# Performance work log

Measured on AMD Instinct MI355X. Metric: run time of the kernel, lower is better.

The kernel has to match this reference:

```python
import jax, jax.numpy as jnp
import numpy as np

D_MODEL = 32
SEQ = 128  # input_dim: each scalar feature is a token


def setup_inputs() -> dict:
    key = jax.random.key(0)
    ks = jax.random.split(key, 11)
    B = 16384
    s = 1.0 / np.sqrt(D_MODEL)
    return {
        "x": jax.random.normal(ks[0], (B, SEQ), dtype=jnp.float32),
        "Wt": jax.random.normal(ks[1], (1, D_MODEL), dtype=jnp.float32),  # token_proj weight (in=1)
        "bt": jax.random.normal(ks[2], (D_MODEL,), dtype=jnp.float32) * 0.02,
        "Wq": jax.random.normal(ks[3], (D_MODEL, D_MODEL), dtype=jnp.float32) * s,
        "bq": jax.random.normal(ks[4], (D_MODEL,), dtype=jnp.float32) * 0.02,
        "Wk": jax.random.normal(ks[5], (D_MODEL, D_MODEL), dtype=jnp.float32) * s,
        "bk": jax.random.normal(ks[6], (D_MODEL,), dtype=jnp.float32) * 0.02,
        "Wv": jax.random.normal(ks[7], (D_MODEL, D_MODEL), dtype=jnp.float32) * s,
        "bv": jax.random.normal(ks[8], (D_MODEL,), dtype=jnp.float32) * 0.02,
        "Wo": jax.random.normal(ks[9], (D_MODEL, 1), dtype=jnp.float32) * s,
        "bo": jax.random.normal(ks[10], (1,), dtype=jnp.float32) * 0.02,
    }


def reference(x, Wt, bt, Wq, bq, Wk, bk, Wv, bv, Wo, bo):
    # x: [B, 128] -> tokens [B, 128, d_model] (each scalar projected from 1 -> d)
    tokens = x[..., None] * Wt[0] + bt  # [B, S, D]
    Q = jnp.einsum("bsd,de->bse", tokens, Wq) + bq
    K = jnp.einsum("bsd,de->bse", tokens, Wk) + bk
    V = jnp.einsum("bsd,de->bse", tokens, Wv) + bv
    scale = jnp.asarray(D_MODEL, x.dtype) ** 0.5
    scores = jnp.einsum("bqd,bkd->bqk", Q, K) / scale  # [B, S, S]
    w = jax.nn.softmax(scores, axis=-1)
    att = jnp.einsum("bqk,bkd->bqd", w, V)  # [B, S, D]
    agg = att.mean(axis=1)  # [B, D]
    risk = agg @ Wo + bo  # [B, 1]
    return risk[:, 0]
```

## Files before the change

kernel.cpp:

```cpp
#include <hip/hip_runtime.h>
#include <hip/hip_bf16.h>

#define SEQ 128
#define DM 32

#define K_LOG2E_2P23 12102203.161561485f
#define SCHRAUDOLPH_C 1064985472.0f
#define INV_SQRT_D 0.17677669529663687f


template <bool CLAMP>
__device__ __forceinline__ void row_loop(const float4* __restrict__ row4,
                                         float T0, float M0, float T1, float M1,
                                         float& s0, float& sxw0,
                                         float& s1, float& sxw1) {
#pragma unroll
    for (int k4 = 0; k4 < SEQ / 4; ++k4) {
        const float4 xv = row4[k4];
#pragma unroll
        for (int j = 0; j < 4; ++j) {
            const float xk = (j == 0) ? xv.x : (j == 1) ? xv.y : (j == 2) ? xv.z : xv.w;
            float v0 = fmaf(T0, xk, M0);
            float v1 = fmaf(T1, xk, M1);
            if (CLAMP) {
                v0 = fmaxf(v0, 0.0f);
                v1 = fmaxf(v1, 0.0f);
            }
            const float e0 = __int_as_float((int)v0);
            const float e1 = __int_as_float((int)v1);
            s0 += e0; sxw0 = fmaf(e0, xk, sxw0);
            s1 += e1; sxw1 = fmaf(e1, xk, sxw1);
        }
    }
}

#define WAVES_PER_BLOCK 4
#define ROWS_PER_WAVE 2

__global__ __launch_bounds__(256) void attn_fused_kernel(
        const float* __restrict__ x,
        const float* __restrict__ Wt, const float* __restrict__ bt,
        const float* __restrict__ Wq, const float* __restrict__ bq,
        const float* __restrict__ Wk,
        const float* __restrict__ Wv, const float* __restrict__ bv,
        const float* __restrict__ Wo, const float* __restrict__ bo,
        float* __restrict__ out, int B) {
    __shared__ float sx[WAVES_PER_BLOCK][ROWS_PER_WAVE][SEQ];

    const int wave = threadIdx.x >> 6;
    const int lane = threadIdx.x & 63;
    const int wg = blockIdx.x * WAVES_PER_BLOCK + wave;
    int b0 = wg * ROWS_PER_WAVE;
    int b1 = b0 + 1;
    if (b0 >= B) b0 = B - 1;
    if (b1 >= B) b1 = B - 1;

    const float* xr0 = x + (size_t)b0 * SEQ;
    const float* xr1 = x + (size_t)b1 * SEQ;
    const float x00 = xr0[lane];
    const float x01 = xr0[lane + 64];
    const float x10 = xr1[lane];
    const float x11 = xr1[lane + 64];

    const int e  = lane & 31;
    const int dh = lane >> 5;
    float qw = 0.f, qb = 0.f, kw = 0.f, vw = 0.f, vb = 0.f;
#pragma unroll
    for (int i = 0; i < 16; ++i) {
        const int d = dh * 16 + i;
        const float wt  = Wt[d];
        const float bb  = bt[d];
        const float wqe = Wq[d * DM + e];
        const float wke = Wk[d * DM + e];
        const float wve = Wv[d * DM + e];
        qw = fmaf(wt, wqe, qw); qb = fmaf(bb, wqe, qb);
        kw = fmaf(wt, wke, kw);
        vw = fmaf(wt, wve, vw); vb = fmaf(bb, wve, vb);
    }
    qw += __shfl_xor(qw, 32); qb += __shfl_xor(qb, 32);
    kw += __shfl_xor(kw, 32);
    vw += __shfl_xor(vw, 32); vb += __shfl_xor(vb, 32);
    qb += bq[e];
    vb += bv[e];
    const float wo = Wo[e];
    float pa  = qw * kw;
    float pc  = qb * kw;
    float pal = vw * wo;
    float pbe = vb * wo;
#pragma unroll
    for (int off = 32; off > 0; off >>= 1) {
        pa  += __shfl_xor(pa,  off);
        pc  += __shfl_xor(pc,  off);
        pal += __shfl_xor(pal, off);
        pbe += __shfl_xor(pbe, off);
    }
    const float A     = pa * (0.5f * INV_SQRT_D * K_LOG2E_2P23);
    const float C     = pc * (0.5f * INV_SQRT_D * K_LOG2E_2P23);
    const float alpha = pal * 0.5f;
    const float beta  = fmaf(pbe, 0.5f, bo[0]);
    const float absA = fabsf(A), absC = fabsf(C);

#pragma unroll
    for (int r = 0; r < ROWS_PER_WAVE; ++r) {
        const float x0 = r ? x10 : x00;
        const float x1 = r ? x11 : x01;
        const int b    = r ? b1 : b0;

        sx[wave][r][lane]      = x0;
        sx[wave][r][lane + 64] = x1;

        float mx = fmaxf(x0, x1);
        float mn = fminf(x0, x1);
#pragma unroll
        for (int off = 32; off > 0; off >>= 1) {
            mx = fmaxf(mx, __shfl_xor(mx, off));
            mn = fminf(mn, __shfl_xor(mn, off));
        }

        const float T0 = fmaf(A, x0, C);
        const float T1 = fmaf(A, x1, C);
        const float m0 = fmaxf(T0 * mx, T0 * mn);
        const float m1 = fmaxf(T1 * mx, T1 * mn);
        const float M0 = SCHRAUDOLPH_C - m0;
        const float M1 = SCHRAUDOLPH_C - m1;

        float s0 = 0.f, sxw0 = 0.f, s1 = 0.f, sxw1 = 0.f;
        const float4* row4 = (const float4*)sx[wave][r];

        const float maxabs = fmaxf(fabsf(mx), fabsf(mn));
        const float tmax = fmaf(absA, maxabs, absC);
        if (tmax * (mx - mn) < 1.0e9f) {
            row_loop<false>(row4, T0, M0, T1, M1, s0, sxw0, s1, sxw1);
        } else {
            row_loop<true>(row4, T0, M0, T1, M1, s0, sxw0, s1, sxw1);
        }

        float msum = sxw0 * __builtin_amdgcn_rcpf(s0) +
                     sxw1 * __builtin_amdgcn_rcpf(s1);
#pragma unroll
        for (int off = 32; off > 0; off >>= 1)
            msum += __shfl_xor(msum, off);

        if (lane == 0)
            out[b] = fmaf(alpha, msum * (1.0f / 128.0f), beta);
    }
}

extern "C" void kernel_launch(void* const* d_in, const int* in_sizes, int n_in,
                              void* d_out, int out_size, void* d_ws, size_t ws_size,
                              hipStream_t stream) {
    const float* x  = (const float*)d_in[0];
    const float* Wt = (const float*)d_in[1];
    const float* bt = (const float*)d_in[2];
    const float* Wq = (const float*)d_in[3];
    const float* bq = (const float*)d_in[4];
    const float* Wk = (const float*)d_in[5];
    const float* Wv = (const float*)d_in[7];
    const float* bv = (const float*)d_in[8];
    const float* Wo = (const float*)d_in[9];
    const float* bo = (const float*)d_in[10];
    float* out = (float*)d_out;

    const int B = in_sizes[0] / SEQ;

    const int rows_per_block = WAVES_PER_BLOCK * ROWS_PER_WAVE;
    const int grid = (B + rows_per_block - 1) / rows_per_block;
    attn_fused_kernel<<<grid, 256, 0, stream>>>(x, Wt, bt, Wq, bq, Wk,
                                                Wv, bv, Wo, bo, out, B);
}
```

Before: 99.28 us.

## Use 1024-thread blocks, one row per wave, share weight constants via LDS

```diff
diff --git a/kernel.cpp b/kernel.cpp
--- a/kernel.cpp
+++ b/kernel.cpp
@@ -34,10 +34,9 @@
     }
 }
 
-#define WAVES_PER_BLOCK 4
-#define ROWS_PER_WAVE 2
+#define WAVES_PER_BLOCK 16
 
-__global__ __launch_bounds__(256) void attn_fused_kernel(
+__global__ __launch_bounds__(1024, 8) void attn_fused_kernel(
         const float* __restrict__ x,
         const float* __restrict__ Wt, const float* __restrict__ bt,
         const float* __restrict__ Wq, const float* __restrict__ bq,
@@ -45,105 +44,102 @@
         const float* __restrict__ Wv, const float* __restrict__ bv,
         const float* __restrict__ Wo, const float* __restrict__ bo,
         float* __restrict__ out, int B) {
-    __shared__ float sx[WAVES_PER_BLOCK][ROWS_PER_WAVE][SEQ];
+    __shared__ float sx[WAVES_PER_BLOCK][SEQ];
+    __shared__ float sconsts[4];
 
     const int wave = threadIdx.x >> 6;
     const int lane = threadIdx.x & 63;
-    const int wg = blockIdx.x * WAVES_PER_BLOCK + wave;
-    int b0 = wg * ROWS_PER_WAVE;
-    int b1 = b0 + 1;
-    if (b0 >= B) b0 = B - 1;
-    if (b1 >= B) b1 = B - 1;
+    int b = blockIdx.x * WAVES_PER_BLOCK + wave;
+    if (b >= B) b = B - 1;
 
-    const float* xr0 = x + (size_t)b0 * SEQ;
-    const float* xr1 = x + (size_t)b1 * SEQ;
-    const float x00 = xr0[lane];
-    const float x01 = xr0[lane + 64];
-    const float x10 = xr1[lane];
-    const float x11 = xr1[lane + 64];
+    const float* xr = x + (size_t)b * SEQ;
+    const float x0 = xr[lane];
+    const float x1 = xr[lane + 64];
+    sx[wave][lane]      = x0;
+    sx[wave][lane + 64] = x1;
 
-    const int e  = lane & 31;
-    const int dh = lane >> 5;
-    float qw = 0.f, qb = 0.f, kw = 0.f, vw = 0.f, vb = 0.f;
-#pragma unroll
-    for (int i = 0; i < 16; ++i) {
-        const int d = dh * 16 + i;
-        const float wt  = Wt[d];
-        const float bb  = bt[d];
-        const float wqe = Wq[d * DM + e];
-        const float wke = Wk[d * DM + e];
-        const float wve = Wv[d * DM + e];
-        qw = fmaf(wt, wqe, qw); qb = fmaf(bb, wqe, qb);
-        kw = fmaf(wt, wke, kw);
-        vw = fmaf(wt, wve, vw); vb = fmaf(bb, wve, vb);
-    }
-    qw += __shfl_xor(qw, 32); qb += __shfl_xor(qb, 32);
-    kw += __shfl_xor(kw, 32);
-    vw += __shfl_xor(vw, 32); vb += __shfl_xor(vb, 32);
-    qb += bq[e];
-    vb += bv[e];
-    const float wo = Wo[e];
-    float pa  = qw * kw;
-    float pc  = qb * kw;
-    float pal = vw * wo;
-    float pbe = vb * wo;
+    float mx = fmaxf(x0, x1);
+    float mn = fminf(x0, x1);
 #pragma unroll
     for (int off = 32; off > 0; off >>= 1) {
-        pa  += __shfl_xor(pa,  off);
-        pc  += __shfl_xor(pc,  off);
-        pal += __shfl_xor(pal, off);
-        pbe += __shfl_xor(pbe, off);
+        mx = fmaxf(mx, __shfl_xor(mx, off));
+        mn = fminf(mn, __shfl_xor(mn, off));
     }
-    const float A     = pa * (0.5f * INV_SQRT_D * K_LOG2E_2P23);
-    const float C     = pc * (0.5f * INV_SQRT_D * K_LOG2E_2P23);
-    const float alpha = pal * 0.5f;
-    const float beta  = fmaf(pbe, 0.5f, bo[0]);
-    const float absA = fabsf(A), absC = fabsf(C);
 
+    if (wave == 0) {
+        const int e  = lane & 31;
+        const int dh = lane >> 5;
+        float qw = 0.f, qb = 0.f, kw = 0.f, vw = 0.f, vb = 0.f;
 #pragma unroll
-    for (int r = 0; r < ROWS_PER_WAVE; ++r) {
-        const float x0 = r ? x10 : x00;
-        const float x1 = r ? x11 : x01;
-        const int b    = r ? b1 : b0;
-
-        sx[wave][r][lane]      = x0;
-        sx[wave][r][lane + 64] = x1;
-
-        float mx = fmaxf(x0, x1);
-        float mn = fminf(x0, x1);
+        for (int i = 0; i < 16; ++i) {
+            const int d = dh * 16 + i;
+            const float wt  = Wt[d];
+            const float bb  = bt[d];
+            const float wqe = Wq[d * DM + e];
+            const float wke = Wk[d * DM + e];
+            const float wve = Wv[d * DM + e];
+            qw = fmaf(wt, wqe, qw); qb = fmaf(bb, wqe, qb);
+            kw = fmaf(wt, wke, kw);
+            vw = fmaf(wt, wve, vw); vb = fmaf(bb, wve, vb);
+        }
+        qw += __shfl_xor(qw, 32); qb += __shfl_xor(qb, 32);
+        kw += __shfl_xor(kw, 32);
+        vw += __shfl_xor(vw, 32); vb += __shfl_xor(vb, 32);
+        qb += bq[e];
+        vb += bv[e];
+        const float wo = Wo[e];
+        float pa  = qw * kw;
+        float pc  = qb * kw;
+        float pal = vw * wo;
+        float pbe = vb * wo;
 #pragma unroll
         for (int off = 32; off > 0; off >>= 1) {
-            mx = fmaxf(mx, __shfl_xor(mx, off));
-            mn = fminf(mn, __shfl_xor(mn, off));
+            pa  += __shfl_xor(pa,  off);
+            pc  += __shfl_xor(pc,  off);
+            pal += __shfl_xor(pal, off);
+            pbe += __shfl_xor(pbe, off);
         }
+        if (lane == 0) {
+            sconsts[0] = pa * (0.5f * INV_SQRT_D * K_LOG2E_2P23);
+            sconsts[1] = pc * (0.5f * INV_SQRT_D * K_LOG2E_2P23);
+            sconsts[2] = pal * 0.5f;
+            sconsts[3] = fmaf(pbe, 0.5f, bo[0]);
+        }
+    }
 
-        const float T0 = fmaf(A, x0, C);
-        const float T1 = fmaf(A, x1, C);
-        const float m0 = fmaxf(T0 * mx, T0 * mn);
-        const float m1 = fmaxf(T1 * mx, T1 * mn);
-        const float M0 = SCHRAUDOLPH_C - m0;
-        const float M1 = SCHRAUDOLPH_C - m1;
+    __syncthreads();
 
-        float s0 = 0.f, sxw0 = 0.f, s1 = 0.f, sxw1 = 0.f;
-        const float4* row4 = (const float4*)sx[wave][r];
+    const float A     = sconsts[0];
+    const float C     = sconsts[1];
+    const float alpha = sconsts[2];
+    const float beta  = sconsts[3];
 
-        const float maxabs = fmaxf(fabsf(mx), fabsf(mn));
-        const float tmax = fmaf(absA, maxabs, absC);
-        if (tmax * (mx - mn) < 1.0e9f) {
-            row_loop<false>(row4, T0, M0, T1, M1, s0, sxw0, s1, sxw1);
-        } else {
-            row_loop<true>(row4, T0, M0, T1, M1, s0, sxw0, s1, sxw1);
-        }
+    const float T0 = fmaf(A, x0, C);
+    const float T1 = fmaf(A, x1, C);
+    const float m0 = fmaxf(T0 * mx, T0 * mn);
+    const float m1 = fmaxf(T1 * mx, T1 * mn);
+    const float M0 = SCHRAUDOLPH_C - m0;
+    const float M1 = SCHRAUDOLPH_C - m1;
 
-        float msum = sxw0 * __builtin_amdgcn_rcpf(s0) +
-                     sxw1 * __builtin_amdgcn_rcpf(s1);
+    float s0 = 0.f, sxw0 = 0.f, s1 = 0.f, sxw1 = 0.f;
+    const float4* row4 = (const float4*)sx[wave];
+
+    const float maxabs = fmaxf(fabsf(mx), fabsf(mn));
+    const float tmax = fmaf(fabsf(A), maxabs, fabsf(C));
+    if (tmax * (mx - mn) < 1.0e9f) {
+        row_loop<false>(row4, T0, M0, T1, M1, s0, sxw0, s1, sxw1);
+    } else {
+        row_loop<true>(row4, T0, M0, T1, M1, s0, sxw0, s1, sxw1);
+    }
+
+    float msum = sxw0 * __builtin_amdgcn_rcpf(s0) +
+                 sxw1 * __builtin_amdgcn_rcpf(s1);
 #pragma unroll
-        for (int off = 32; off > 0; off >>= 1)
-            msum += __shfl_xor(msum, off);
+    for (int off = 32; off > 0; off >>= 1)
+        msum += __shfl_xor(msum, off);
 
-        if (lane == 0)
-            out[b] = fmaf(alpha, msum * (1.0f / 128.0f), beta);
-    }
+    if (lane == 0)
+        out[b] = fmaf(alpha, msum * (1.0f / 128.0f), beta);
 }
 
 extern "C" void kernel_launch(void* const* d_in, const int* in_sizes, int n_in,
@@ -163,8 +159,7 @@
 
     const int B = in_sizes[0] / SEQ;
 
-    const int rows_per_block = WAVES_PER_BLOCK * ROWS_PER_WAVE;
-    const int grid = (B + rows_per_block - 1) / rows_per_block;
-    attn_fused_kernel<<<grid, 256, 0, stream>>>(x, Wt, bt, Wq, bq, Wk,
-                                                Wv, bv, Wo, bo, out, B);
+    const int grid = (B + WAVES_PER_BLOCK - 1) / WAVES_PER_BLOCK;
+    attn_fused_kernel<<<grid, 1024, 0, stream>>>(x, Wt, bt, Wq, bq, Wk,
+                                                 Wv, bv, Wo, bo, out, B);
 }
```

New measurement: 98.07 us. No clear change (-1.2%).
